# Kernel optimization log

Hardware: AMD Instinct MI355X
Metric: run time of the kernel (lower is better)

## Reference

```python
import jax, jax.numpy as jnp
import numpy as np

DIM = 96
GROUPS = 8          # SPPE factor
CG = DIM // GROUPS  # channels per SPPE group = 12
D_STATE = 16
D_CONV = 4
D_INNER = 2 * DIM   # expand=2
DT_RANK = 6         # ceil(96/16)
EPS = 1e-5


def setup_inputs() -> dict:
    key = jax.random.key(0)
    ks = jax.random.split(key, 16)
    def w(k, shape, s=0.02):
        return (jax.random.normal(k, shape) * s).astype(jnp.float32)
    z = lambda *s: jnp.zeros(s, jnp.float32)
    inp = {
        "x": jax.random.normal(ks[0], (2, DIM, 32, 32, 32), dtype=jnp.float32),
        # SPPE params
        "sppe_c1_w": w(ks[1], (CG, CG)), "sppe_c1_b": z(CG),
        "sppe_c3_w": w(ks[2], (CG, CG, 3, 3, 3)), "sppe_c3_b": z(CG),
        "sppe_gn_w": jnp.ones((CG,), jnp.float32), "sppe_gn_b": z(CG),
        # Mamba params (mamba_ssm defaults: proj biases False, conv bias True)
        "in_proj_w": w(ks[3], (2 * D_INNER, DIM)),
        "conv1d_w": w(ks[4], (D_INNER, D_CONV), 0.1), "conv1d_b": z(D_INNER),
        "x_proj_w": w(ks[5], (DT_RANK + 2 * D_STATE, D_INNER)),
        "dt_proj_w": w(ks[6], (D_INNER, DT_RANK), 0.1),
        "dt_proj_b": w(ks[7], (D_INNER,), 0.1),
        "A_log": jnp.log(jnp.tile(jnp.arange(1, D_STATE + 1, dtype=jnp.float32), (D_INNER, 1))),
        "ssm_D": jnp.ones((D_INNER,), jnp.float32),
        "out_proj_w": w(ks[8], (DIM, D_INNER)),
        # MlpChannel params (1x1 Conv3d == pointwise linear over channels)
        "mlp_fc1_w": w(ks[9], (4 * DIM, DIM)), "mlp_fc1_b": z(4 * DIM),
        "mlp_fc2_w": w(ks[10], (DIM, 4 * DIM)), "mlp_fc2_b": z(DIM),
    }
    return inp


def _inorm(x):
    # InstanceNorm3d (affine=False, biased var) over spatial dims per (b,c)
    m = jnp.mean(x, axis=(2, 3, 4), keepdims=True)
    v = jnp.var(x, axis=(2, 3, 4), keepdims=True)
    return (x - m) * jax.lax.rsqrt(v + EPS)


def _sppe(x, c1_w, c1_b, c3_w, c3_b, gn_w, gn_b):
    b, c, h, w, d = x.shape
    bg = b * GROUPS
    gx = x.reshape(bg, CG, h, w, d)
    # directional pools, each ending as (bg, CG, axis_len, 1, 1)
    x_h = jnp.mean(gx, axis=(3, 4), keepdims=True)                      # (bg,CG,h,1,1)
    x_w = jnp.mean(gx, axis=(2, 4), keepdims=True).transpose(0, 1, 3, 2, 4)
    x_d = jnp.mean(gx, axis=(2, 3), keepdims=True).transpose(0, 1, 4, 3, 2)
    hwd = jnp.concatenate([x_h, x_w, x_d], axis=2)[..., 0, 0]          # (bg,CG,h+w+d)
    hwd = jnp.einsum("oc,bcn->bon", c1_w, hwd) + c1_b[:, None]
    g_h = jax.nn.sigmoid(hwd[:, :, :h])[:, :, :, None, None]           # (bg,CG,h,1,1)
    g_w = jax.nn.sigmoid(hwd[:, :, h:h + w])[:, :, None, :, None]      # (bg,CG,1,w,1)
    g_d = jax.nn.sigmoid(hwd[:, :, h + w:])[:, :, None, None, :]       # (bg,CG,1,1,d)
    gated = gx * g_h * g_w * g_d
    # GroupNorm(num_groups=CG, num_channels=CG) == per-channel norm + affine
    gm = jnp.mean(gated, axis=(2, 3, 4), keepdims=True)
    gv = jnp.var(gated, axis=(2, 3, 4), keepdims=True)
    x1 = (gated - gm) * jax.lax.rsqrt(gv + EPS)
    x1 = x1 * gn_w[:, None, None, None] + gn_b[:, None, None, None]
    x2 = jax.lax.conv_general_dilated(
        gx, c3_w, (1, 1, 1), [(1, 1)] * 3,
        dimension_numbers=("NCDHW", "OIDHW", "NCDHW")) + c3_b[:, None, None, None]
    n = h * w * d
    x11 = jax.nn.softmax(jnp.mean(x1, axis=(2, 3, 4)), axis=-1)        # (bg,CG)
    x21 = jax.nn.softmax(jnp.mean(x2, axis=(2, 3, 4)), axis=-1)
    x12 = x2.reshape(bg, CG, n)
    x22 = x1.reshape(bg, CG, n)
    weights = (jnp.einsum("bc,bcn->bn", x11, x12)
               + jnp.einsum("bc,bcn->bn", x21, x22)).reshape(bg, 1, h, w, d)
    return (gx * jax.nn.sigmoid(weights)).reshape(b, c, h, w, d)


def _mamba(seq, in_proj_w, conv1d_w, conv1d_b, x_proj_w, dt_proj_w, dt_proj_b,
           A_log, ssm_D, out_proj_w):
    # seq: (B, L, DIM)
    B, L, _ = seq.shape
    xz = seq @ in_proj_w.T                       # (B,L,2*E)
    xm, zg = jnp.split(xz, 2, axis=-1)
    # depthwise causal conv1d along L
    xc = jax.lax.conv_general_dilated(
        xm.transpose(0, 2, 1), conv1d_w[:, None, :], (1,), [(D_CONV - 1, 0)],
        dimension_numbers=("NCH", "OIH", "NCH"), feature_group_count=D_INNER)
    xc = jax.nn.silu((xc + conv1d_b[:, None]).transpose(0, 2, 1))  # (B,L,E)
    dbl = xc @ x_proj_w.T                         # (B,L,DT_RANK+2N)
    dt = jax.nn.softplus(dbl[..., :DT_RANK] @ dt_proj_w.T + dt_proj_b)  # (B,L,E)
    Bm = dbl[..., DT_RANK:DT_RANK + D_STATE]      # (B,L,N)
    Cm = dbl[..., DT_RANK + D_STATE:]             # (B,L,N)
    A = -jnp.exp(A_log)                           # (E,N)

    def step(h, t):
        dt_t, b_t, c_t, x_t = t                   # (B,E),(B,N),(B,N),(B,E)
        dA = jnp.exp(dt_t[:, :, None] * A)        # (B,E,N)
        h = h * dA + (dt_t * x_t)[:, :, None] * b_t[:, None, :]
        return h, jnp.einsum("ben,bn->be", h, c_t)

    h0 = jnp.zeros((B, D_INNER, D_STATE), seq.dtype)
    _, ys = jax.lax.scan(step, h0, (dt.transpose(1, 0, 2), Bm.transpose(1, 0, 2),
                                    Cm.transpose(1, 0, 2), xc.transpose(1, 0, 2)))
    y = ys.transpose(1, 0, 2) + xc * ssm_D
    y = y * jax.nn.silu(zg)
    return y @ out_proj_w.T                       # (B,L,DIM)


def reference(x, sppe_c1_w, sppe_c1_b, sppe_c3_w, sppe_c3_b, sppe_gn_w, sppe_gn_b,
              in_proj_w, conv1d_w, conv1d_b, x_proj_w, dt_proj_w, dt_proj_b,
              A_log, ssm_D, out_proj_w, mlp_fc1_w, mlp_fc1_b, mlp_fc2_w, mlp_fc2_b):
    y_sppe = _sppe(x, sppe_c1_w, sppe_c1_b, sppe_c3_w, sppe_c3_b, sppe_gn_w, sppe_gn_b)
    B, C, H, W, Dd = x.shape
    L = H * W * Dd
    seq = _inorm(x).reshape(B, C, L).transpose(0, 2, 1)           # (B,L,C)
    out = _mamba(seq, in_proj_w, conv1d_w, conv1d_b, x_proj_w,
                 dt_proj_w, dt_proj_b, A_log, ssm_D, out_proj_w)
    xo = out.transpose(0, 2, 1).reshape(B, C, H, W, Dd)
    xo = _inorm(xo) * y_sppe
    t = jnp.einsum("oc,bchwd->bohwd", mlp_fc1_w, xo) + mlp_fc1_b[:, None, None, None]
    t = jax.nn.gelu(t, approximate=False)
    t = jnp.einsum("oc,bchwd->bohwd", mlp_fc2_w, t) + mlp_fc2_b[:, None, None, None]
    return t + x
```

## Files before the change

### kernel.cpp

```cpp
#include <hip/hip_runtime.h>
#include <math.h>

#define NSPA 32768
#define TCH 32
#define NCH 1024
#define EPS 1e-5f

#define ST_MEAN   0
#define ST_RSTD   192
#define ST_GM     384
#define ST_GRSTD  576
#define ST_X2SUM  768
#define ST_XH     1024
#define ST_XW     7168
#define ST_XD     13312
#define ST_GATE   19456
#define ST_MEAN2  38400
#define ST_RSTD2  38592
#define ST_WT     40960

__device__ __forceinline__ float sigmoidf_(float x){ return 1.f/(1.f+__expf(-x)); }
__device__ __forceinline__ float siluf_(float x){ return x/(1.f+__expf(-x)); }
__device__ __forceinline__ float geluf_(float x){ return 0.5f*x*(1.f+erff(x*0.70710678118654752f)); }
__device__ __forceinline__ float softplusf_(float x){ return fmaxf(x,0.f) + log1pf(__expf(-fabsf(x))); }

__global__ void k_prep(const float* __restrict__ c3w, const float* __restrict__ W1,
                       const float* __restrict__ W2, const float* __restrict__ Wip,
                       const float* __restrict__ xpw,
                       float* __restrict__ wt, float* __restrict__ W1t,
                       float* __restrict__ W2t, float* __restrict__ Wipt,
                       float* __restrict__ xpWt) {
  int idx = blockIdx.x*256 + threadIdx.x;
  if (idx < 3888) {
    int co = idx/324, r = idx%324;
    wt[r*12+co] = c3w[co*324+r];
  } else if (idx < 40752) {
    int i = idx-3888; int k = i/384, h = i%384;
    W1t[i] = W1[(size_t)h*96+k];
  } else if (idx < 77616) {
    int i = idx-40752; int k = i/96, o = i%96;
    W2t[i] = W2[(size_t)o*384+k];
  } else if (idx < 114480) {
    int i = idx-77616; int k = i/384, r = i%384;
    Wipt[i] = Wip[(size_t)r*96+k];
  } else if (idx < 123696) {
    int i = idx-114480; int e = i/48, o = i%48;
    float v = 0.f;
    if (o < 38) { int row = (o<32)? (o+6) : (o-32); v = xpw[(size_t)row*192+e]; }
    xpWt[i] = v;
  }
}

__global__ void k_stats(const float* __restrict__ x, float* __restrict__ st) {
  int bc = blockIdx.x;
  int t = threadIdx.x;
  __shared__ float xh_s[32], xw_s[32], xd_s[32], red[16], red2[16];
  if (t < 32) { xh_s[t]=0.f; xw_s[t]=0.f; xd_s[t]=0.f; }
  __syncthreads();
  const float* px = x + (size_t)bc*NSPA;
  float s=0.f, s2=0.f;
  for (int it=0; it<32; ++it) {
    float v = px[it*1024 + t];
    s += v; s2 += v*v;
    float wv = v;
    #pragma unroll
    for (int m=32;m>=1;m>>=1) wv += __shfl_xor(wv,m);
    if ((t&63)==0) atomicAdd(&xh_s[it], wv);
  }
  atomicAdd(&xw_s[(t>>5)&31], s);
  atomicAdd(&xd_s[t&31], s);
  float rs=s, rs2=s2;
  #pragma unroll
  for (int m=32;m>=1;m>>=1){ rs += __shfl_xor(rs,m); rs2 += __shfl_xor(rs2,m); }
  if ((t&63)==0){ red[t>>6]=rs; red2[t>>6]=rs2; }
  __syncthreads();
  if (t==0){
    float S=0.f,S2=0.f;
    for (int w=0;w<16;w++){ S+=red[w]; S2+=red2[w]; }
    float mn = S/(float)NSPA;
    float var = S2/(float)NSPA - mn*mn;
    st[ST_MEAN+bc] = mn;
    st[ST_RSTD+bc] = rsqrtf(var+EPS);
  }
  if (t<32){
    st[ST_XH + bc*32 + t] = xh_s[t]*(1.f/1024.f);
    st[ST_XW + bc*32 + t] = xw_s[t]*(1.f/1024.f);
    st[ST_XD + bc*32 + t] = xd_s[t]*(1.f/1024.f);
  }
}

__global__ void k_gates(const float* __restrict__ c1w, const float* __restrict__ c1b,
                        float* __restrict__ st) {
  int bg = blockIdx.x; int b = bg>>3; int g = bg&7;
  for (int i = threadIdx.x; i < 12*96; i += 128) {
    int co = i/96, pos = i%96;
    float acc = c1b[co];
    for (int cg=0; cg<12; ++cg) {
      int bc = b*96 + g*12 + cg;
      float hv;
      if (pos < 32)      hv = st[ST_XH + bc*32 + pos];
      else if (pos < 64) hv = st[ST_XW + bc*32 + pos-32];
      else               hv = st[ST_XD + bc*32 + pos-64];
      acc += c1w[co*12+cg]*hv;
    }
    st[ST_GATE + bg*1152 + i] = sigmoidf_(acc);
  }
}

__global__ void k_gated(const float* __restrict__ x, float* __restrict__ gated,
                        float* __restrict__ st) {
  int bc = blockIdx.x; int bg = bc/12; int cg = bc%12;
  int t = threadIdx.x;
  const float* gate = st + ST_GATE + bg*1152 + cg*96;
  float gw = gate[32 + (t>>5)];
  float gd = gate[64 + (t&31)];
  const float* px = x + (size_t)bc*NSPA;
  float* pg = gated + (size_t)bc*NSPA;
  __shared__ float red[16], red2[16];
  float s=0.f, s2=0.f;
  for (int it=0; it<32; ++it) {
    float gh = gate[it];
    float v = px[it*1024+t]*gh*gw*gd;
    pg[it*1024+t] = v;
    s += v; s2 += v*v;
  }
  #pragma unroll
  for (int m=32;m>=1;m>>=1){ s += __shfl_xor(s,m); s2 += __shfl_xor(s2,m); }
  if ((t&63)==0){ red[t>>6]=s; red2[t>>6]=s2; }
  __syncthreads();
  if (t==0){
    float S=0.f,S2=0.f;
    for (int w=0;w<16;w++){ S+=red[w]; S2+=red2[w]; }
    float mn = S/(float)NSPA;
    float var = S2/(float)NSPA - mn*mn;
    st[ST_GM+bc] = mn;
    st[ST_GRSTD+bc] = rsqrtf(var+EPS);
  }
}

__global__ void k_conv3(const float* __restrict__ x, const float* __restrict__ wt,
                        const float* __restrict__ c3b, float* __restrict__ x2,
                        float* __restrict__ st) {
  __shared__ float sl[3][12*324];
  __shared__ float ssum[12];
  int bg = blockIdx.z;
  int w0 = (blockIdx.x & 1)*16, d0 = (blockIdx.x >> 1)*16;
  int h0 = blockIdx.y*4;
  int tid = threadIdx.x;
  if (tid < 12) ssum[tid] = 0.f;

  const float* xb = x + (size_t)bg*12*NSPA;

  auto load_slab = [&](int hh, int s){
    for (int i=tid; i<3888; i+=256){
      int ci = i/324, r = i%324;
      int lw = r/18, ld = r%18;
      int gw = w0-1+lw, gd = d0-1+ld;
      float v = 0.f;
      if ((unsigned)hh<32u && (unsigned)gw<32u && (unsigned)gd<32u)
        v = xb[(size_t)ci*NSPA + hh*1024 + gw*32 + gd];
      sl[s][i] = v;
    }
  };

  load_slab(h0-1, ((h0-1)%3+3)%3);
  load_slab(h0,   h0%3);
  load_slab(h0+1, (h0+1)%3);
  __syncthreads();

  int w = tid>>4, d = tid&15;
  int base_wd = w*18 + d;
  float b0v=c3b[0],b1v=c3b[1],b2v=c3b[2],b3v=c3b[3],b4v=c3b[4],b5v=c3b[5],
        b6v=c3b[6],b7v=c3b[7],b8v=c3b[8],b9v=c3b[9],b10v=c3b[10],b11v=c3b[11];

  for (int it=0; it<4; ++it){
    int h = h0 + it;
    const float* sm1 = sl[((h-1)%3+3)%3];
    const float* s00 = sl[h%3];
    const float* sp1 = sl[(h+1)%3];
    float acc[12];
    acc[0]=b0v; acc[1]=b1v; acc[2]=b2v; acc[3]=b3v; acc[4]=b4v; acc[5]=b5v;
    acc[6]=b6v; acc[7]=b7v; acc[8]=b8v; acc[9]=b9v; acc[10]=b10v; acc[11]=b11v;
    for (int ci=0; ci<12; ++ci){
      const float* w_ci = wt + ci*324;
      #pragma unroll
      for (int kh=0;kh<3;kh++){
        const float* sp = (kh==0)? sm1 : ((kh==1)? s00 : sp1);
        const float* srow = sp + ci*324 + base_wd;
        #pragma unroll
        for (int kw=0;kw<3;kw++){
          #pragma unroll
          for (int kd=0;kd<3;kd++){
            float v = srow[kw*18 + kd];
            const float4* wp = (const float4*)(w_ci + (kh*9+kw*3+kd)*12);
            float4 wa = wp[0], wb = wp[1], wc = wp[2];
            acc[0]=fmaf(wa.x,v,acc[0]); acc[1]=fmaf(wa.y,v,acc[1]);
            acc[2]=fmaf(wa.z,v,acc[2]); acc[3]=fmaf(wa.w,v,acc[3]);
            acc[4]=fmaf(wb.x,v,acc[4]); acc[5]=fmaf(wb.y,v,acc[5]);
            acc[6]=fmaf(wb.z,v,acc[6]); acc[7]=fmaf(wb.w,v,acc[7]);
            acc[8]=fmaf(wc.x,v,acc[8]); acc[9]=fmaf(wc.y,v,acc[9]);
            acc[10]=fmaf(wc.z,v,acc[10]); acc[11]=fmaf(wc.w,v,acc[11]);
          }
        }
      }
    }
    int l = h*1024 + (w0+w)*32 + (d0+d);
    #pragma unroll
    for (int co=0;co<12;co++){
      float r = acc[co];
      x2[(size_t)(bg*12+co)*NSPA + l] = r;
      float rv = r;
      #pragma unroll
      for (int m=32;m>=1;m>>=1) rv += __shfl_xor(rv,m);
      if ((tid&63)==0) atomicAdd(&ssum[co], rv);
    }
    __syncthreads();
    if (it<3){
      load_slab(h+2, (h+2)%3);
      __syncthreads();
    }
  }
  if (tid<12) atomicAdd(&st[ST_X2SUM + bg*12 + tid], ssum[tid]);
}

__global__ void k_sppe_out(const float* __restrict__ gated,
                           const float* __restrict__ x2, const float* __restrict__ gnw,
                           const float* __restrict__ gnb, const float* __restrict__ st,
                           float* __restrict__ sigb) {
  int bg = blockIdx.y; int b = bg>>3; int g = bg&7;
  __shared__ float x11s[12], alphas[12], betasum_s;
  if (threadIdx.x==0){
    float m1=-1e30f, m2=-1e30f;
    float mu2[12];
    for (int cg=0;cg<12;cg++){
      int bc=b*96+g*12+cg;
      mu2[cg] = st[ST_X2SUM+bc]*(1.f/(float)NSPA);
      m1 = fmaxf(m1, gnb[cg]); m2 = fmaxf(m2, mu2[cg]);
    }
    float e1[12], e2[12]; float s1=0.f, s2=0.f;
    for (int cg=0;cg<12;cg++){ e1[cg]=expf(gnb[cg]-m1); s1+=e1[cg];
                               e2[cg]=expf(mu2[cg]-m2); s2+=e2[cg]; }
    float bs=0.f;
    for (int cg=0;cg<12;cg++){
      int bc=b*96+g*12+cg;
      float x11 = e1[cg]/s1;
      float x21 = e2[cg]/s2;
      x11s[cg]=x11;
      float gr = st[ST_GRSTD+bc], gm = st[ST_GM+bc];
      alphas[cg] = x21*gr*gnw[cg];
      bs += x21*(gnb[cg] - gm*gr*gnw[cg]);
    }
    betasum_s = bs;
  }
  __syncthreads();
  int l = blockIdx.x*256 + threadIdx.x;
  float wsum = betasum_s;
  int bc0 = b*96+g*12;
  for (int cg=0;cg<12;cg++){
    size_t off = (size_t)(bc0+cg)*NSPA + l;
    wsum += x11s[cg]*x2[off] + alphas[cg]*gated[off];
  }
  sigb[(size_t)bg*NSPA + l] = sigmoidf_(wsum);
}

__global__ void k_front(const float* __restrict__ x, const float* __restrict__ Wipt,
                        const float* __restrict__ Wip,
                        const float* __restrict__ cw, const float* __restrict__ cb,
                        const float* __restrict__ st,
                        float* __restrict__ xc_t, float* __restrict__ zg_t) {
  __shared__ float As[96*64];
  __shared__ float outS[48*65];
  __shared__ float haloS[3*192];
  int b = blockIdx.y; int l0 = blockIdx.x*64; int tid = threadIdx.x;
  const float* mean = st + ST_MEAN + b*96;
  const float* rstd = st + ST_RSTD + b*96;
  for (int i=tid;i<96*64;i+=256){
    int k=i>>6, l=i&63;
    As[i] = (x[((size_t)b*96+k)*NSPA + l0+l]-mean[k])*rstd[k];
  }
  for (int i=tid;i<576;i+=256){
    int j=i/192, e=i%192;
    int t = l0-3+j;
    float s = 0.f;
    if (t >= 0){
      const float* wr = Wip + (size_t)e*96;
      for (int k=0;k<96;k++)
        s += wr[k]*(x[((size_t)b*96+k)*NSPA + t]-mean[k])*rstd[k];
    }
    haloS[i] = s;
  }
  __syncthreads();
  int wv = __builtin_amdgcn_readfirstlane(tid>>6);
  int lane = tid&63;
  for (int p=0;p<8;++p){
    int r0 = p*48 + wv*12;
    float acc[12];
    #pragma unroll
    for (int j=0;j<12;j++) acc[j]=0.f;
    for (int k=0;k<96;k++){
      float a = As[k*64+lane];
      const float4* wp = (const float4*)&Wipt[(size_t)k*384 + r0];
      float4 w0=wp[0],w1=wp[1],w2=wp[2];
      acc[0]=fmaf(w0.x,a,acc[0]);  acc[1]=fmaf(w0.y,a,acc[1]);
      acc[2]=fmaf(w0.z,a,acc[2]);  acc[3]=fmaf(w0.w,a,acc[3]);
      acc[4]=fmaf(w1.x,a,acc[4]);  acc[5]=fmaf(w1.y,a,acc[5]);
      acc[6]=fmaf(w1.z,a,acc[6]);  acc[7]=fmaf(w1.w,a,acc[7]);
      acc[8]=fmaf(w2.x,a,acc[8]);  acc[9]=fmaf(w2.y,a,acc[9]);
      acc[10]=fmaf(w2.z,a,acc[10]); acc[11]=fmaf(w2.w,a,acc[11]);
    }
    if (p) __syncthreads();
    if (p < 4){
      #pragma unroll
      for (int j=0;j<12;j++){
        int e = r0 + j;
        float v = acc[j];
        float vm1 = __shfl_up(v,1);
        float vm2 = __shfl_up(v,2);
        float vm3 = __shfl_up(v,3);
        if (lane==0) vm1 = haloS[2*192+e];
        if (lane<=1) vm2 = haloS[(1+lane)*192+e];
        if (lane<=2) vm3 = haloS[(0+lane)*192+e];
        float4 w4 = *(const float4*)&cw[e*4];
        float r_ = cb[e] + w4.x*vm3 + w4.y*vm2 + w4.z*vm1 + w4.w*v;
        outS[(wv*12+j)*65 + lane] = siluf_(r_);
      }
    } else {
      #pragma unroll
      for (int j=0;j<12;j++) outS[(wv*12+j)*65 + lane] = acc[j];
    }
    __syncthreads();
    float* dst = (p<4) ? xc_t : zg_t;
    int e0 = (p<4) ? p*48 : (p-4)*48;
    for (int i=tid; i<64*12; i+=256){
      int l = i/12, q = i%12;
      float4 v;
      v.x = outS[(q*4+0)*65 + l];
      v.y = outS[(q*4+1)*65 + l];
      v.z = outS[(q*4+2)*65 + l];
      v.w = outS[(q*4+3)*65 + l];
      *(float4*)&dst[((size_t)b*NSPA + l0+l)*192 + e0 + q*4] = v;
    }
  }
}

__global__ void k_gemm_xp(const float* __restrict__ A, const float* __restrict__ xpWt,
                          float* __restrict__ dbl_t) {
  __shared__ float As[96*65];
  __shared__ float dblS[48*65];
  int b = blockIdx.y; int l0 = blockIdx.x*64; int tid = threadIdx.x;
  int wv = __builtin_amdgcn_readfirstlane(tid>>6);
  int lane = tid&63;
  int o0 = wv*12;
  float acc[12];
  #pragma unroll
  for (int j=0;j<12;j++) acc[j]=0.f;
  for (int h=0;h<2;++h){
    if (h) __syncthreads();
    for (int i=tid;i<64*24;i+=256){
      int l=i/24, q=i%24;
      float4 v = *(const float4*)&A[((size_t)b*NSPA + l0+l)*192 + h*96 + q*4];
      As[(q*4+0)*65+l]=v.x; As[(q*4+1)*65+l]=v.y;
      As[(q*4+2)*65+l]=v.z; As[(q*4+3)*65+l]=v.w;
    }
    __syncthreads();
    for (int k=0;k<96;k++){
      float a = As[k*65+lane];
      const float4* wp = (const float4*)&xpWt[(size_t)(h*96+k)*48 + o0];
      float4 w0=wp[0],w1=wp[1],w2=wp[2];
      acc[0]=fmaf(w0.x,a,acc[0]);  acc[1]=fmaf(w0.y,a,acc[1]);
      acc[2]=fmaf(w0.z,a,acc[2]);  acc[3]=fmaf(w0.w,a,acc[3]);
      acc[4]=fmaf(w1.x,a,acc[4]);  acc[5]=fmaf(w1.y,a,acc[5]);
      acc[6]=fmaf(w1.z,a,acc[6]);  acc[7]=fmaf(w1.w,a,acc[7]);
      acc[8]=fmaf(w2.x,a,acc[8]);  acc[9]=fmaf(w2.y,a,acc[9]);
      acc[10]=fmaf(w2.z,a,acc[10]); acc[11]=fmaf(w2.w,a,acc[11]);
    }
  }
  __syncthreads();
  #pragma unroll
  for (int j=0;j<12;j++) dblS[(o0+j)*65 + lane] = acc[j];
  __syncthreads();
  for (int i=tid;i<64*10;i+=256){
    int l=i/10, q=i%10;
    float4 v;
    v.x = dblS[(q*4+0)*65+l]; v.y = dblS[(q*4+1)*65+l];
    v.z = dblS[(q*4+2)*65+l]; v.w = dblS[(q*4+3)*65+l];
    *(float4*)&dbl_t[((size_t)b*NSPA + l0+l)*40 + q*4] = v;
  }
}

__global__ void k_gemm_out(const float* __restrict__ A, const float* __restrict__ W,
                           float* __restrict__ out) {
  __shared__ float As[192*64];
  int b = blockIdx.y; int l0 = blockIdx.x*64; int tid = threadIdx.x;
  for (int f=tid; f<48*64; f+=256){
    int l = f&63, kq = f>>6;
    float4 v = *(const float4*)&A[((size_t)b*NSPA + l0+l)*192 + kq*4];
    As[(kq*4+0)*64+l]=v.x; As[(kq*4+1)*64+l]=v.y;
    As[(kq*4+2)*64+l]=v.z; As[(kq*4+3)*64+l]=v.w;
  }
  __syncthreads();
  int l4=(tid&15)*4; int og=tid>>4;
  for (int o0=og*4; o0<96; o0+=64){
    float acc[16];
    #pragma unroll
    for (int i=0;i<16;i++) acc[i]=0.f;
    for (int k=0;k<192;k++){
      float4 a = *(const float4*)&As[k*64+l4];
      #pragma unroll
      for (int j=0;j<4;j++){
        float wv = W[(size_t)(o0+j)*192+k];
        acc[j*4+0]+=wv*a.x; acc[j*4+1]+=wv*a.y; acc[j*4+2]+=wv*a.z; acc[j*4+3]+=wv*a.w;
      }
    }
    #pragma unroll
    for (int j=0;j<4;j++){
      int o=o0+j;
      float4 r; r.x=acc[j*4+0]; r.y=acc[j*4+1]; r.z=acc[j*4+2]; r.w=acc[j*4+3];
      *(float4*)&out[((size_t)b*96+o)*NSPA + l0+l4] = r;
    }
  }
}

__global__ void k_scanA(const float* __restrict__ xc_t, const float* __restrict__ dbl_t,
                        const float* __restrict__ dtw, const float* __restrict__ dtb,
                        const float* __restrict__ A_log,
                        float* __restrict__ P, float* __restrict__ hend) {
  int b = blockIdx.y, ch = blockIdx.x; int e = threadIdx.x;
  float An[16];
  #pragma unroll
  for (int n=0;n<16;n++) An[n] = -__expf(A_log[e*16+n]);
  float wdt[6];
  #pragma unroll
  for (int j=0;j<6;j++) wdt[j]=dtw[e*6+j];
  float bdt = dtb[e];
  const float* drow = dbl_t + ((size_t)b*NSPA + (size_t)ch*TCH)*40;
  const float* xrow = xc_t + ((size_t)b*NSPA + (size_t)ch*TCH)*192 + e;
  float h[16], Pp[16];
  #pragma unroll
  for (int n=0;n<16;n++){ h[n]=0.f; Pp[n]=1.f; }
  for (int l=0;l<TCH;l++){
    const float* u = drow + l*40;
    float4 b0=*(const float4*)(u+0), b1=*(const float4*)(u+4),
           b2=*(const float4*)(u+8), b3=*(const float4*)(u+12);
    float4 d4=*(const float4*)(u+32);
    float2 d2=*(const float2*)(u+36);
    float x = xrow[(size_t)l*192];
    float pre = bdt + wdt[0]*d4.x + wdt[1]*d4.y + wdt[2]*d4.z
                    + wdt[3]*d4.w + wdt[4]*d2.x + wdt[5]*d2.y;
    float dte = softplusf_(pre);
    float dtx = dte*x;
    float Bv[16] = {b0.x,b0.y,b0.z,b0.w, b1.x,b1.y,b1.z,b1.w,
                    b2.x,b2.y,b2.z,b2.w, b3.x,b3.y,b3.z,b3.w};
    #pragma unroll
    for (int n=0;n<16;n++){
      float a = __expf(dte*An[n]);
      Pp[n] *= a;
      h[n] = h[n]*a + dtx*Bv[n];
    }
  }
  size_t o = (((size_t)b*NCH+ch)*192+e)*16;
  #pragma unroll
  for (int q=0;q<4;q++){
    float4 rp; rp.x=Pp[q*4+0]; rp.y=Pp[q*4+1]; rp.z=Pp[q*4+2]; rp.w=Pp[q*4+3];
    *(float4*)&P[o+q*4] = rp;
    float4 rh; rh.x=h[q*4+0]; rh.y=h[q*4+1]; rh.z=h[q*4+2]; rh.w=h[q*4+3];
    *(float4*)&hend[o+q*4] = rh;
  }
}

__global__ void k_scanB(const float* __restrict__ P, const float* __restrict__ hend,
                        float* __restrict__ Hs) {
  __shared__ float sP[16][64], sH[16][64];
  int b = blockIdx.y;
  int rl = threadIdx.x & 63;
  int cg = threadIdx.x >> 6;
  int r  = blockIdx.x*64 + rl;
  size_t base = (size_t)b*NCH*3072 + r;
  int c0 = cg*64;
  float Pl = 1.f, hl = 0.f;
  for (int c=c0; c<c0+64; ++c){
    size_t idx = base + (size_t)c*3072;
    float Pc = P[idx], Hc = hend[idx];
    hl = fmaf(Pc, hl, Hc);
    Pl *= Pc;
  }
  sP[cg][rl] = Pl; sH[cg][rl] = hl;
  __syncthreads();
  float H = 0.f;
  for (int g=0; g<cg; ++g) H = fmaf(sP[g][rl], H, sH[g][rl]);
  for (int c=c0; c<c0+64; ++c){
    size_t idx = base + (size_t)c*3072;
    float Pc = P[idx], Hc = hend[idx];
    Hs[idx] = H;
    H = fmaf(Pc, H, Hc);
  }
}

__global__ void k_scanC(const float* xc_t, const float* __restrict__ dbl_t,
                        const float* __restrict__ dtw, const float* __restrict__ dtb,
                        const float* __restrict__ A_log, const float* __restrict__ Hs,
                        const float* __restrict__ ssm_D, const float* __restrict__ zg_t,
                        float* y_t) {
  int b = blockIdx.y, ch = blockIdx.x; int e = threadIdx.x;
  float An[16];
  #pragma unroll
  for (int n=0;n<16;n++) An[n] = -__expf(A_log[e*16+n]);
  float wdt[6];
  #pragma unroll
  for (int j=0;j<6;j++) wdt[j]=dtw[e*6+j];
  float bdt = dtb[e];
  float Dv = ssm_D[e];
  const float* drow = dbl_t + ((size_t)b*NSPA + (size_t)ch*TCH)*40;
  const float* xrow = xc_t + ((size_t)b*NSPA + (size_t)ch*TCH)*192 + e;
  const float* zrow = zg_t + ((size_t)b*NSPA + (size_t)ch*TCH)*192 + e;
  float* yrow = y_t + ((size_t)b*NSPA + (size_t)ch*TCH)*192 + e;
  float h[16];
  size_t ho = (((size_t)b*NCH+ch)*192+e)*16;
  #pragma unroll
  for (int q=0;q<4;q++){
    float4 hv = *(const float4*)&Hs[ho+q*4];
    h[q*4+0]=hv.x; h[q*4+1]=hv.y; h[q*4+2]=hv.z; h[q*4+3]=hv.w;
  }
  for (int l=0;l<TCH;l++){
    const float* u = drow + l*40;
    float4 b0=*(const float4*)(u+0), b1=*(const float4*)(u+4),
           b2=*(const float4*)(u+8), b3=*(const float4*)(u+12);
    float4 c0=*(const float4*)(u+16), c1=*(const float4*)(u+20),
           c2=*(const float4*)(u+24), c3=*(const float4*)(u+28);
    float4 d4=*(const float4*)(u+32);
    float2 d2=*(const float2*)(u+36);
    float x = xrow[(size_t)l*192];
    float z = zrow[(size_t)l*192];
    float pre = bdt + wdt[0]*d4.x + wdt[1]*d4.y + wdt[2]*d4.z
                    + wdt[3]*d4.w + wdt[4]*d2.x + wdt[5]*d2.y;
    float dte = softplusf_(pre);
    float dtx = dte*x;
    float Bv[16] = {b0.x,b0.y,b0.z,b0.w, b1.x,b1.y,b1.z,b1.w,
                    b2.x,b2.y,b2.z,b2.w, b3.x,b3.y,b3.z,b3.w};
    float Cv[16] = {c0.x,c0.y,c0.z,c0.w, c1.x,c1.y,c1.z,c1.w,
                    c2.x,c2.y,c2.z,c2.w, c3.x,c3.y,c3.z,c3.w};
    float yp = 0.f;
    #pragma unroll
    for (int n=0;n<16;n++){
      float a = __expf(dte*An[n]);
      h[n] = h[n]*a + dtx*Bv[n];
      yp += h[n]*Cv[n];
    }
    yrow[(size_t)l*192] = (yp + x*Dv)*siluf_(z);
  }
}

__global__ void k_stats2(const float* __restrict__ outb, float* __restrict__ st) {
  int bc = blockIdx.x; int t = threadIdx.x;
  const float* p = outb + (size_t)bc*NSPA;
  float s=0.f, s2=0.f;
  for (int i=t;i<NSPA;i+=256){ float v=p[i]; s+=v; s2+=v*v; }
  __shared__ float red[4], red2[4];
  #pragma unroll
  for (int m=32;m>=1;m>>=1){ s += __shfl_xor(s,m); s2 += __shfl_xor(s2,m); }
  if ((t&63)==0){ red[t>>6]=s; red2[t>>6]=s2; }
  __syncthreads();
  if (t==0){
    float S=red[0]+red[1]+red[2]+red[3];
    float S2=red2[0]+red2[1]+red2[2]+red2[3];
    float mn=S/(float)NSPA; float var=S2/(float)NSPA-mn*mn;
    st[ST_MEAN2+bc]=mn; st[ST_RSTD2+bc]=rsqrtf(var+EPS);
  }
}

__global__ void k_mlpF(const float* __restrict__ outb, const float* __restrict__ sigb,
                       const float* __restrict__ st,
                       const float* __restrict__ W1t, const float* __restrict__ b1,
                       const float* __restrict__ W2t, const float* __restrict__ b2,
                       const float* __restrict__ x, float* __restrict__ dout) {
  __shared__ float xoS[96*64];
  __shared__ float hidS[2][32*64];
  int b = blockIdx.y; int l0 = blockIdx.x*64; int tid = threadIdx.x;
  for (int i=tid;i<96*64;i+=256){
    int k=i>>6, l=i&63;
    size_t off = ((size_t)b*96+k)*NSPA + l0+l;
    float sv = sigb[((size_t)(b*8 + k/12))*NSPA + l0+l];
    xoS[i] = (outb[off]-st[ST_MEAN2+b*96+k])*st[ST_RSTD2+b*96+k]*x[off]*sv;
  }
  __syncthreads();
  int wv = __builtin_amdgcn_readfirstlane(tid >> 6);
  int lane = tid & 63;
  float acc2[24];
  #pragma unroll
  for (int i=0;i<24;i++) acc2[i]=0.f;
  int o0 = wv*24;

  for (int c=0; c<12; ++c){
    int h0 = c*32 + wv*8;
    float acc1[8];
    #pragma unroll
    for (int i=0;i<8;i++) acc1[i]=0.f;
    for (int k=0;k<96;k++){
      float a = xoS[k*64 + lane];
      const float4* wp = (const float4*)&W1t[(size_t)k*384 + h0];
      float4 w0=wp[0], w1=wp[1];
      acc1[0]=fmaf(w0.x,a,acc1[0]);  acc1[1]=fmaf(w0.y,a,acc1[1]);
      acc1[2]=fmaf(w0.z,a,acc1[2]);  acc1[3]=fmaf(w0.w,a,acc1[3]);
      acc1[4]=fmaf(w1.x,a,acc1[4]);  acc1[5]=fmaf(w1.y,a,acc1[5]);
      acc1[6]=fmaf(w1.z,a,acc1[6]);  acc1[7]=fmaf(w1.w,a,acc1[7]);
    }
    float* hb = hidS[c&1];
    #pragma unroll
    for (int j=0;j<8;j++)
      hb[(wv*8+j)*64 + lane] = geluf_(acc1[j] + b1[h0+j]);
    __syncthreads();
    for (int k2=0;k2<32;k2++){
      float a = hb[k2*64 + lane];
      int kg = c*32 + k2;
      const float4* wp = (const float4*)&W2t[(size_t)kg*96 + o0];
      float4 w0=wp[0], w1=wp[1], w2=wp[2], w3=wp[3], w4=wp[4], w5=wp[5];
      acc2[0]=fmaf(w0.x,a,acc2[0]);  acc2[1]=fmaf(w0.y,a,acc2[1]);
      acc2[2]=fmaf(w0.z,a,acc2[2]);  acc2[3]=fmaf(w0.w,a,acc2[3]);
      acc2[4]=fmaf(w1.x,a,acc2[4]);  acc2[5]=fmaf(w1.y,a,acc2[5]);
      acc2[6]=fmaf(w1.z,a,acc2[6]);  acc2[7]=fmaf(w1.w,a,acc2[7]);
      acc2[8]=fmaf(w2.x,a,acc2[8]);  acc2[9]=fmaf(w2.y,a,acc2[9]);
      acc2[10]=fmaf(w2.z,a,acc2[10]); acc2[11]=fmaf(w2.w,a,acc2[11]);
      acc2[12]=fmaf(w3.x,a,acc2[12]); acc2[13]=fmaf(w3.y,a,acc2[13]);
      acc2[14]=fmaf(w3.z,a,acc2[14]); acc2[15]=fmaf(w3.w,a,acc2[15]);
      acc2[16]=fmaf(w4.x,a,acc2[16]); acc2[17]=fmaf(w4.y,a,acc2[17]);
      acc2[18]=fmaf(w4.z,a,acc2[18]); acc2[19]=fmaf(w4.w,a,acc2[19]);
      acc2[20]=fmaf(w5.x,a,acc2[20]); acc2[21]=fmaf(w5.y,a,acc2[21]);
      acc2[22]=fmaf(w5.z,a,acc2[22]); acc2[23]=fmaf(w5.w,a,acc2[23]);
    }
  }
  #pragma unroll
  for (int j=0;j<24;j++){
    int o = o0 + j;
    size_t off = ((size_t)b*96+o)*NSPA + l0 + lane;
    dout[off] = acc2[j] + b2[o] + x[off];
  }
}

extern "C" void kernel_launch(void* const* d_in, const int* in_sizes, int n_in,
                              void* d_out, int out_size, void* d_ws, size_t ws_size,
                              hipStream_t stream) {
  const float* x        = (const float*)d_in[0];
  const float* c1w      = (const float*)d_in[1];
  const float* c1b      = (const float*)d_in[2];
  const float* c3w      = (const float*)d_in[3];
  const float* c3b      = (const float*)d_in[4];
  const float* gnw      = (const float*)d_in[5];
  const float* gnb      = (const float*)d_in[6];
  const float* in_proj  = (const float*)d_in[7];
  const float* conv1dw  = (const float*)d_in[8];
  const float* conv1db  = (const float*)d_in[9];
  const float* xprojw   = (const float*)d_in[10];
  const float* dtw      = (const float*)d_in[11];
  const float* dtb      = (const float*)d_in[12];
  const float* A_log    = (const float*)d_in[13];
  const float* ssm_D    = (const float*)d_in[14];
  const float* outprojw = (const float*)d_in[15];
  const float* W1       = (const float*)d_in[16];
  const float* b1       = (const float*)d_in[17];
  const float* W2       = (const float*)d_in[18];
  const float* b2       = (const float*)d_in[19];
  float* dout = (float*)d_out;

  float* ws = (float*)d_ws;
  const size_t o_st = 0;
  const size_t o_A  = 65536;
  const size_t o_B  = o_A + 12582912;
  const size_t o_C  = o_B + 12582912;
  const size_t o_D  = o_C + 12582912;
  const size_t o_E  = o_D + 6291456;
  const size_t o_F  = o_E + 6291456;
  float* st    = ws + o_st;
  float* P     = ws + o_A;
  float* Hs    = ws + o_A + 6291456;
  float* zg_t  = ws + o_B;
  float* xc_t  = ws + o_C;
  float* y_t   = ws + o_C;
  float* gated = ws + o_D;
  float* dbl_t = ws + o_D;
  float* x2b   = ws + o_E;
  float* hendb = ws + o_E;
  float* outb  = ws + o_E;
  float* W1t   = ws + o_F + 0;
  float* W2t   = ws + o_F + 40960;
  float* Wipt  = ws + o_F + 81920;
  float* xpWt  = ws + o_F + 122880;
  float* sigb  = ws + o_F + 200704;
  float* wtb   = st + ST_WT;

  hipMemsetAsync(st, 0, 65536*sizeof(float), stream);

  k_prep<<<484, 256, 0, stream>>>(c3w, W1, W2, in_proj, xprojw,
                                  wtb, W1t, W2t, Wipt, xpWt);
  k_stats<<<192, 1024, 0, stream>>>(x, st);
  k_gates<<<16, 128, 0, stream>>>(c1w, c1b, st);
  k_gated<<<192, 1024, 0, stream>>>(x, gated, st);
  k_conv3<<<dim3(4,8,16), 256, 0, stream>>>(x, wtb, c3b, x2b, st);
  k_sppe_out<<<dim3(128,16), 256, 0, stream>>>(gated, x2b, gnw, gnb, st, sigb);
  k_front<<<dim3(512,2), 256, 0, stream>>>(x, Wipt, in_proj, conv1dw, conv1db,
                                           st, xc_t, zg_t);
  k_gemm_xp<<<dim3(512,2), 256, 0, stream>>>(xc_t, xpWt, dbl_t);
  k_scanA<<<dim3(NCH,2), 192, 0, stream>>>(xc_t, dbl_t, dtw, dtb, A_log, P, hendb);
  k_scanB<<<dim3(48,2), 1024, 0, stream>>>(P, hendb, Hs);
  k_scanC<<<dim3(NCH,2), 192, 0, stream>>>(xc_t, dbl_t, dtw, dtb, A_log, Hs,
                                           ssm_D, zg_t, y_t);
  k_gemm_out<<<dim3(512,2), 256, 0, stream>>>(y_t, outprojw, outb);
  k_stats2<<<192, 256, 0, stream>>>(outb, st);
  k_mlpF<<<dim3(512,2), 256, 0, stream>>>(outb, sigb, st, W1t, b1, W2t, b2, x, dout);
}
```

Before: 876.4 us.

## Fuse SPPE gating and stats into conv3 and output-norm stats into out GEMM

```diff
diff --git a/kernel.cpp b/kernel.cpp
--- a/kernel.cpp
+++ b/kernel.cpp
@@ -8,8 +8,6 @@
 
 #define ST_MEAN   0
 #define ST_RSTD   192
-#define ST_GM     384
-#define ST_GRSTD  576
 #define ST_X2SUM  768
 #define ST_XH     1024
 #define ST_XW     7168
@@ -17,6 +15,10 @@
 #define ST_GATE   19456
 #define ST_MEAN2  38400
 #define ST_RSTD2  38592
+#define ST_OSUM   38784
+#define ST_OSQ    38976
+#define ST_GSUM   39168
+#define ST_GSQ    39360
 #define ST_WT     40960
 
 __device__ __forceinline__ float sigmoidf_(float x){ return 1.f/(1.f+__expf(-x)); }
@@ -107,47 +109,26 @@
   }
 }
 
-__global__ void k_gated(const float* __restrict__ x, float* __restrict__ gated,
-                        float* __restrict__ st) {
-  int bc = blockIdx.x; int bg = bc/12; int cg = bc%12;
-  int t = threadIdx.x;
-  const float* gate = st + ST_GATE + bg*1152 + cg*96;
-  float gw = gate[32 + (t>>5)];
-  float gd = gate[64 + (t&31)];
-  const float* px = x + (size_t)bc*NSPA;
-  float* pg = gated + (size_t)bc*NSPA;
-  __shared__ float red[16], red2[16];
-  float s=0.f, s2=0.f;
-  for (int it=0; it<32; ++it) {
-    float gh = gate[it];
-    float v = px[it*1024+t]*gh*gw*gd;
-    pg[it*1024+t] = v;
-    s += v; s2 += v*v;
-  }
-  #pragma unroll
-  for (int m=32;m>=1;m>>=1){ s += __shfl_xor(s,m); s2 += __shfl_xor(s2,m); }
-  if ((t&63)==0){ red[t>>6]=s; red2[t>>6]=s2; }
-  __syncthreads();
-  if (t==0){
-    float S=0.f,S2=0.f;
-    for (int w=0;w<16;w++){ S+=red[w]; S2+=red2[w]; }
-    float mn = S/(float)NSPA;
-    float var = S2/(float)NSPA - mn*mn;
-    st[ST_GM+bc] = mn;
-    st[ST_GRSTD+bc] = rsqrtf(var+EPS);
-  }
-}
-
 __global__ void k_conv3(const float* __restrict__ x, const float* __restrict__ wt,
-                        const float* __restrict__ c3b, float* __restrict__ x2,
-                        float* __restrict__ st) {
+                        const float* __restrict__ c3b, const float* __restrict__ gnb,
+                        float* __restrict__ ww, float* __restrict__ st) {
   __shared__ float sl[3][12*324];
   __shared__ float ssum[12];
+  __shared__ float x11S[12];
+  __shared__ float gateS[1152];
   int bg = blockIdx.z;
   int w0 = (blockIdx.x & 1)*16, d0 = (blockIdx.x >> 1)*16;
   int h0 = blockIdx.y*4;
   int tid = threadIdx.x;
   if (tid < 12) ssum[tid] = 0.f;
+  if (tid == 0){
+    float m=-1e30f;
+    for (int i=0;i<12;i++) m=fmaxf(m,gnb[i]);
+    float e[12]; float s=0.f;
+    for (int i=0;i<12;i++){ e[i]=expf(gnb[i]-m); s+=e[i]; }
+    for (int i=0;i<12;i++) x11S[i]=e[i]/s;
+  }
+  for (int i=tid;i<1152;i+=256) gateS[i] = st[ST_GATE + bg*1152 + i];
 
   const float* xb = x + (size_t)bg*12*NSPA;
 
@@ -172,6 +153,14 @@
   int base_wd = w*18 + d;
   float b0v=c3b[0],b1v=c3b[1],b2v=c3b[2],b3v=c3b[3],b4v=c3b[4],b5v=c3b[5],
         b6v=c3b[6],b7v=c3b[7],b8v=c3b[8],b9v=c3b[9],b10v=c3b[10],b11v=c3b[11];
+
+  float gwd[12];
+  #pragma unroll
+  for (int ci=0;ci<12;ci++)
+    gwd[ci] = gateS[ci*96+32+(w0+w)] * gateS[ci*96+64+(d0+d)];
+  float sg[12], sg2[12];
+  #pragma unroll
+  for (int ci=0;ci<12;ci++){ sg[ci]=0.f; sg2[ci]=0.f; }
 
   for (int it=0; it<4; ++it){
     int h = h0 + it;
@@ -204,12 +193,19 @@
         }
       }
     }
+    float wwv = 0.f;
+    #pragma unroll
+    for (int ci=0;ci<12;ci++){
+      float xc = s00[ci*324 + base_wd + 19];
+      float gv = xc * gwd[ci] * gateS[ci*96 + h];
+      sg[ci] += gv; sg2[ci] += gv*gv;
+      wwv = fmaf(x11S[ci], acc[ci], wwv);
+    }
     int l = h*1024 + (w0+w)*32 + (d0+d);
+    ww[(size_t)bg*NSPA + l] = wwv;
     #pragma unroll
     for (int co=0;co<12;co++){
-      float r = acc[co];
-      x2[(size_t)(bg*12+co)*NSPA + l] = r;
-      float rv = r;
+      float rv = acc[co];
       #pragma unroll
       for (int m=32;m>=1;m>>=1) rv += __shfl_xor(rv,m);
       if ((tid&63)==0) atomicAdd(&ssum[co], rv);
@@ -221,44 +217,54 @@
     }
   }
   if (tid<12) atomicAdd(&st[ST_X2SUM + bg*12 + tid], ssum[tid]);
-}
-
-__global__ void k_sppe_out(const float* __restrict__ gated,
-                           const float* __restrict__ x2, const float* __restrict__ gnw,
-                           const float* __restrict__ gnb, const float* __restrict__ st,
-                           float* __restrict__ sigb) {
+  #pragma unroll
+  for (int ci=0;ci<12;ci++){
+    float a = sg[ci], a2 = sg2[ci];
+    #pragma unroll
+    for (int m=32;m>=1;m>>=1){ a += __shfl_xor(a,m); a2 += __shfl_xor(a2,m); }
+    if ((tid&63)==0){
+      atomicAdd(&st[ST_GSUM + bg*12 + ci], a);
+      atomicAdd(&st[ST_GSQ  + bg*12 + ci], a2);
+    }
+  }
+}
+
+__global__ void k_sppe_out(const float* __restrict__ x, const float* __restrict__ ww,
+                           const float* __restrict__ gnw, const float* __restrict__ gnb,
+                           const float* __restrict__ st, float* __restrict__ sigb) {
   int bg = blockIdx.y; int b = bg>>3; int g = bg&7;
-  __shared__ float x11s[12], alphas[12], betasum_s;
+  __shared__ float alphaS[12], betasum_s;
+  __shared__ float gateS[1152];
+  for (int i=threadIdx.x;i<1152;i+=256) gateS[i] = st[ST_GATE + bg*1152 + i];
   if (threadIdx.x==0){
-    float m1=-1e30f, m2=-1e30f;
-    float mu2[12];
+    float m2=-1e30f; float mu2[12];
     for (int cg=0;cg<12;cg++){
       int bc=b*96+g*12+cg;
       mu2[cg] = st[ST_X2SUM+bc]*(1.f/(float)NSPA);
-      m1 = fmaxf(m1, gnb[cg]); m2 = fmaxf(m2, mu2[cg]);
-    }
-    float e1[12], e2[12]; float s1=0.f, s2=0.f;
-    for (int cg=0;cg<12;cg++){ e1[cg]=expf(gnb[cg]-m1); s1+=e1[cg];
-                               e2[cg]=expf(mu2[cg]-m2); s2+=e2[cg]; }
+      m2 = fmaxf(m2, mu2[cg]);
+    }
+    float e2[12]; float s2=0.f;
+    for (int cg=0;cg<12;cg++){ e2[cg]=expf(mu2[cg]-m2); s2+=e2[cg]; }
     float bs=0.f;
     for (int cg=0;cg<12;cg++){
       int bc=b*96+g*12+cg;
-      float x11 = e1[cg]/s1;
       float x21 = e2[cg]/s2;
-      x11s[cg]=x11;
-      float gr = st[ST_GRSTD+bc], gm = st[ST_GM+bc];
-      alphas[cg] = x21*gr*gnw[cg];
+      float gm = st[ST_GSUM+bc]*(1.f/(float)NSPA);
+      float gvar = st[ST_GSQ+bc]*(1.f/(float)NSPA) - gm*gm;
+      float gr = rsqrtf(gvar+EPS);
+      alphaS[cg] = x21*gr*gnw[cg];
       bs += x21*(gnb[cg] - gm*gr*gnw[cg]);
     }
     betasum_s = bs;
   }
   __syncthreads();
   int l = blockIdx.x*256 + threadIdx.x;
-  float wsum = betasum_s;
+  int h = l>>10, w8 = (l>>5)&31, d = l&31;
+  float wsum = betasum_s + ww[(size_t)bg*NSPA + l];
   int bc0 = b*96+g*12;
   for (int cg=0;cg<12;cg++){
-    size_t off = (size_t)(bc0+cg)*NSPA + l;
-    wsum += x11s[cg]*x2[off] + alphas[cg]*gated[off];
+    float G = gateS[cg*96+h]*gateS[cg*96+32+w8]*gateS[cg*96+64+d];
+    wsum = fmaf(alphaS[cg]*G, x[(size_t)(bc0+cg)*NSPA + l], wsum);
   }
   sigb[(size_t)bg*NSPA + l] = sigmoidf_(wsum);
 }
@@ -389,7 +395,7 @@
 }
 
 __global__ void k_gemm_out(const float* __restrict__ A, const float* __restrict__ W,
-                           float* __restrict__ out) {
+                           float* __restrict__ out, float* __restrict__ st) {
   __shared__ float As[192*64];
   int b = blockIdx.y; int l0 = blockIdx.x*64; int tid = threadIdx.x;
   for (int f=tid; f<48*64; f+=256){
@@ -417,8 +423,24 @@
       int o=o0+j;
       float4 r; r.x=acc[j*4+0]; r.y=acc[j*4+1]; r.z=acc[j*4+2]; r.w=acc[j*4+3];
       *(float4*)&out[((size_t)b*96+o)*NSPA + l0+l4] = r;
-    }
-  }
+      float s  = r.x+r.y+r.z+r.w;
+      float s2 = r.x*r.x+r.y*r.y+r.z*r.z+r.w*r.w;
+      #pragma unroll
+      for (int m=8;m>=1;m>>=1){ s += __shfl_xor(s,m); s2 += __shfl_xor(s2,m); }
+      if ((tid&15)==0){
+        atomicAdd(&st[ST_OSUM + b*96 + o], s);
+        atomicAdd(&st[ST_OSQ  + b*96 + o], s2);
+      }
+    }
+  }
+}
+
+__global__ void k_fin(float* __restrict__ st){
+  int t = threadIdx.x;
+  float mn = st[ST_OSUM+t]*(1.f/(float)NSPA);
+  float var = st[ST_OSQ+t]*(1.f/(float)NSPA) - mn*mn;
+  st[ST_MEAN2+t] = mn;
+  st[ST_RSTD2+t] = rsqrtf(var+EPS);
 }
 
 __global__ void k_scanA(const float* __restrict__ xc_t, const float* __restrict__ dbl_t,
@@ -550,31 +572,13 @@
   }
 }
 
-__global__ void k_stats2(const float* __restrict__ outb, float* __restrict__ st) {
-  int bc = blockIdx.x; int t = threadIdx.x;
-  const float* p = outb + (size_t)bc*NSPA;
-  float s=0.f, s2=0.f;
-  for (int i=t;i<NSPA;i+=256){ float v=p[i]; s+=v; s2+=v*v; }
-  __shared__ float red[4], red2[4];
-  #pragma unroll
-  for (int m=32;m>=1;m>>=1){ s += __shfl_xor(s,m); s2 += __shfl_xor(s2,m); }
-  if ((t&63)==0){ red[t>>6]=s; red2[t>>6]=s2; }
-  __syncthreads();
-  if (t==0){
-    float S=red[0]+red[1]+red[2]+red[3];
-    float S2=red2[0]+red2[1]+red2[2]+red2[3];
-    float mn=S/(float)NSPA; float var=S2/(float)NSPA-mn*mn;
-    st[ST_MEAN2+bc]=mn; st[ST_RSTD2+bc]=rsqrtf(var+EPS);
-  }
-}
-
 __global__ void k_mlpF(const float* __restrict__ outb, const float* __restrict__ sigb,
                        const float* __restrict__ st,
                        const float* __restrict__ W1t, const float* __restrict__ b1,
                        const float* __restrict__ W2t, const float* __restrict__ b2,
                        const float* __restrict__ x, float* __restrict__ dout) {
   __shared__ float xoS[96*64];
-  __shared__ float hidS[2][32*64];
+  __shared__ float hidS[64*64];
   int b = blockIdx.y; int l0 = blockIdx.x*64; int tid = threadIdx.x;
   for (int i=tid;i<96*64;i+=256){
     int k=i>>6, l=i&63;
@@ -590,28 +594,32 @@
   for (int i=0;i<24;i++) acc2[i]=0.f;
   int o0 = wv*24;
 
-  for (int c=0; c<12; ++c){
-    int h0 = c*32 + wv*8;
-    float acc1[8];
-    #pragma unroll
-    for (int i=0;i<8;i++) acc1[i]=0.f;
+  for (int c=0; c<6; ++c){
+    int h0 = c*64 + wv*16;
+    float acc1[16];
+    #pragma unroll
+    for (int i=0;i<16;i++) acc1[i]=0.f;
     for (int k=0;k<96;k++){
       float a = xoS[k*64 + lane];
       const float4* wp = (const float4*)&W1t[(size_t)k*384 + h0];
-      float4 w0=wp[0], w1=wp[1];
+      float4 w0=wp[0], w1=wp[1], w2=wp[2], w3=wp[3];
       acc1[0]=fmaf(w0.x,a,acc1[0]);  acc1[1]=fmaf(w0.y,a,acc1[1]);
       acc1[2]=fmaf(w0.z,a,acc1[2]);  acc1[3]=fmaf(w0.w,a,acc1[3]);
       acc1[4]=fmaf(w1.x,a,acc1[4]);  acc1[5]=fmaf(w1.y,a,acc1[5]);
       acc1[6]=fmaf(w1.z,a,acc1[6]);  acc1[7]=fmaf(w1.w,a,acc1[7]);
-    }
-    float* hb = hidS[c&1];
-    #pragma unroll
-    for (int j=0;j<8;j++)
-      hb[(wv*8+j)*64 + lane] = geluf_(acc1[j] + b1[h0+j]);
+      acc1[8]=fmaf(w2.x,a,acc1[8]);  acc1[9]=fmaf(w2.y,a,acc1[9]);
+      acc1[10]=fmaf(w2.z,a,acc1[10]); acc1[11]=fmaf(w2.w,a,acc1[11]);
+      acc1[12]=fmaf(w3.x,a,acc1[12]); acc1[13]=fmaf(w3.y,a,acc1[13]);
+      acc1[14]=fmaf(w3.z,a,acc1[14]); acc1[15]=fmaf(w3.w,a,acc1[15]);
+    }
+    if (c) __syncthreads();
+    #pragma unroll
+    for (int j=0;j<16;j++)
+      hidS[(wv*16+j)*64 + lane] = geluf_(acc1[j] + b1[h0+j]);
     __syncthreads();
-    for (int k2=0;k2<32;k2++){
-      float a = hb[k2*64 + lane];
-      int kg = c*32 + k2;
+    for (int k2=0;k2<64;k2++){
+      float a = hidS[k2*64 + lane];
+      int kg = c*64 + k2;
       const float4* wp = (const float4*)&W2t[(size_t)kg*96 + o0];
       float4 w0=wp[0], w1=wp[1], w2=wp[2], w3=wp[3], w4=wp[4], w5=wp[5];
       acc2[0]=fmaf(w0.x,a,acc2[0]);  acc2[1]=fmaf(w0.y,a,acc2[1]);
@@ -675,9 +683,7 @@
   float* zg_t  = ws + o_B;
   float* xc_t  = ws + o_C;
   float* y_t   = ws + o_C;
-  float* gated = ws + o_D;
   float* dbl_t = ws + o_D;
-  float* x2b   = ws + o_E;
   float* hendb = ws + o_E;
   float* outb  = ws + o_E;
   float* W1t   = ws + o_F + 0;
@@ -685,6 +691,7 @@
   float* Wipt  = ws + o_F + 81920;
   float* xpWt  = ws + o_F + 122880;
   float* sigb  = ws + o_F + 200704;
+  float* wwb   = ws + o_F + 724992;
   float* wtb   = st + ST_WT;
 
   hipMemsetAsync(st, 0, 65536*sizeof(float), stream);
@@ -693,9 +700,8 @@
                                   wtb, W1t, W2t, Wipt, xpWt);
   k_stats<<<192, 1024, 0, stream>>>(x, st);
   k_gates<<<16, 128, 0, stream>>>(c1w, c1b, st);
-  k_gated<<<192, 1024, 0, stream>>>(x, gated, st);
-  k_conv3<<<dim3(4,8,16), 256, 0, stream>>>(x, wtb, c3b, x2b, st);
-  k_sppe_out<<<dim3(128,16), 256, 0, stream>>>(gated, x2b, gnw, gnb, st, sigb);
+  k_conv3<<<dim3(4,8,16), 256, 0, stream>>>(x, wtb, c3b, gnb, wwb, st);
+  k_sppe_out<<<dim3(128,16), 256, 0, stream>>>(x, wwb, gnw, gnb, st, sigb);
   k_front<<<dim3(512,2), 256, 0, stream>>>(x, Wipt, in_proj, conv1dw, conv1db,
                                            st, xc_t, zg_t);
   k_gemm_xp<<<dim3(512,2), 256, 0, stream>>>(xc_t, xpWt, dbl_t);
@@ -703,7 +709,7 @@
   k_scanB<<<dim3(48,2), 1024, 0, stream>>>(P, hendb, Hs);
   k_scanC<<<dim3(NCH,2), 192, 0, stream>>>(xc_t, dbl_t, dtw, dtb, A_log, Hs,
                                            ssm_D, zg_t, y_t);
-  k_gemm_out<<<dim3(512,2), 256, 0, stream>>>(y_t, outprojw, outb);
-  k_stats2<<<192, 256, 0, stream>>>(outb, st);
+  k_gemm_out<<<dim3(512,2), 256, 0, stream>>>(y_t, outprojw, outb, st);
+  k_fin<<<1, 192, 0, stream>>>(st);
   k_mlpF<<<dim3(512,2), 256, 0, stream>>>(outb, sigb, st, W1t, b1, W2t, b2, x, dout);
 }
```

Result: slower. 947.2 us (+8.1%).
